# Performance work log

Measured on AMD Instinct MI355X. Metric: run time of the kernel, lower is better.

## Reference

```python
import jax, jax.numpy as jnp
import numpy as np

B, N_BUG, D_BUG, K, L, P = 2048, 2000, 30, 20, 40, 2
OMEGA_TEMP = 1.0


def setup_inputs() -> dict:
    key = jax.random.key(0)
    ks = jax.random.split(key, 14)
    f = lambda k, s, sc=1.0: sc * jax.random.normal(k, s, dtype=jnp.float32)
    return {
        "x": f(ks[0], (B, N_BUG)),
        "microbe_locs": f(ks[1], (N_BUG, D_BUG)),
        "mu_bug": f(ks[2], (L, D_BUG)),
        "r_bug": jax.random.uniform(ks[3], (L,), dtype=jnp.float32) * 20.0 + 10.0,
        "alpha": f(ks[4], (L, K)),
        "beta": f(ks[5], (K,)),
        "W1": f(ks[6], (K, L, P, 16), 0.5),
        "b1": f(ks[7], (K, L, P, 16), 0.1),
        "W2": f(ks[8], (K, L, P, 16, 16), 0.25),
        "b2": f(ks[9], (K, L, P, 16), 0.1),
        "W3": f(ks[10], (K, L, P, 16, 8), 0.25),
        "b3": f(ks[11], (K, L, P, 8), 0.1),
        "W4": f(ks[12], (K, L, P, 8), 0.35),
        "b4": f(ks[13], (K, L, P), 0.1),
    }


def reference(x, microbe_locs, mu_bug, r_bug, alpha, beta,
              W1, b1, W2, b2, W3, b3, W4, b4):
    # Distance-based soft microbe->cluster assignment (mu/r kernel):
    # kappa[m,l] = ||microbe_locs[m] - mu_bug[l]||^2
    kappa = jnp.sum((microbe_locs[:, None, :] - mu_bug[None, :, :]) ** 2, axis=-1)  # [N_bug, L]
    w_act = jax.nn.sigmoid((r_bug[None, :] - kappa) / OMEGA_TEMP)                  # [N_bug, L]
    g = x @ w_act                                                                   # [B, L] per-cluster microbe sums

    alpha_act = jax.nn.sigmoid(alpha)  # [L, K] soft edge selection

    # NAM: K*L*P independent tiny MLPs 1->16->16->8->1, batched over (k,l,p).
    h1 = jax.nn.elu(g[:, None, :, None, None] * W1[None] + b1[None])          # [B,K,L,P,16]
    h2 = jax.nn.elu(jnp.einsum('bklpi,klpij->bklpj', h1, W2) + b2[None])      # [B,K,L,P,16]
    h3 = jax.nn.elu(jnp.einsum('bklpi,klpij->bklpj', h2, W3) + b3[None])      # [B,K,L,P,8]
    f_out = jnp.einsum('bklpi,klpi->bklp', h3, W4) + b4[None]                 # [B,K,L,P]

    # out[b,k] = beta[k] + sum_l alpha_act[l,k] * sum_p f_out[b,k,l,p]
    out = beta[None, :] + jnp.einsum('bklp,lk->bk', f_out, alpha_act)         # [B,K]
    return out
```

## Files before the change

### kernel.cpp

```cpp
#include <hip/hip_runtime.h>
#include <hip/hip_bf16.h>

#define B_SZ 2048
#define NB   2000
#define DB   30
#define KK   20
#define LL   40
#define PP   2

#define BLOB_F 336

#define GRID_K1 880

typedef _Float16 f16x4 __attribute__((ext_vector_type(4)));
typedef float    f32x4 __attribute__((ext_vector_type(4)));

__device__ __forceinline__ float sigmoidf_fast(float z) {
    return 1.0f / (1.0f + __expf(-z));
}
__device__ __forceinline__ float eluf(float x) {
    return x > 0.0f ? x : (__expf(x) - 1.0f);
}

__global__ __launch_bounds__(256) void k1_prep(
    const float* __restrict__ locs, const float* __restrict__ mu,
    const float* __restrict__ r, const float* __restrict__ alpha,
    const float* __restrict__ beta,
    const float* __restrict__ W1, const float* __restrict__ b1,
    const float* __restrict__ W2, const float* __restrict__ b2,
    const float* __restrict__ W3, const float* __restrict__ b3,
    const float* __restrict__ W4, const float* __restrict__ b4,
    float* __restrict__ w_act, float* __restrict__ blob,
    float* __restrict__ g_T, float* __restrict__ out)
{
    __shared__ float smem[LL * DB + LL];
    const int tid  = threadIdx.x;
    const int bidx = blockIdx.x;
    const int vt   = bidx * 256 + tid;

    for (int j = vt; j < LL * B_SZ; j += GRID_K1 * 256) g_T[j] = 0.0f;

    if (bidx < 320) {
        for (int t = tid; t < LL * DB; t += 256) smem[t] = mu[t];
        if (tid < LL) smem[LL * DB + tid] = r[tid];
        __syncthreads();
        if (vt < NB * LL) {
            int m = vt / LL;
            int l = vt - m * LL;
            float kappa = 0.0f;
            #pragma unroll
            for (int d = 0; d < DB; ++d) {
                float diff = locs[m * DB + d] - smem[l * DB + d];
                kappa += diff * diff;
            }
            w_act[vt] = sigmoidf_fast(smem[LL * DB + l] - kappa);
        }
    } else if (bidx < 720) {
        int vt2 = vt - 320 * 256;
        int bidb = vt2 >> 6;
        int t = vt2 & 63;
        int k = bidb / (PP * LL);
        int rem = bidb - k * (PP * LL);
        int p = rem / LL;
        int l = rem - p * LL;
        int iw = (k * LL + l) * PP + p;
        int n = t & 15, q = t >> 4;
        float* o = blob + (size_t)bidb * BLOB_F;
        float aact = sigmoidf_fast(alpha[l * KK + k]);
        if (t < 16) {
            o[t]      = W1[iw * 16 + t];
            o[16 + t] = b1[iw * 16 + t];
            o[32 + t] = b2[iw * 16 + t];
            o[48 + t] = (t < 8) ? b3[iw * 8 + t] : 0.0f;
            o[64 + t] = (t < 8) ? W4[iw * 8 + t] * aact : 0.0f;
        }
        _Float16* w2a = (_Float16*)(o + 80);
        #pragma unroll
        for (int j = 0; j < 4; ++j)
            w2a[t * 4 + j] = (_Float16)W2[iw * 256 + (4 * q + j) * 16 + n];
        _Float16* w3a = (_Float16*)(o + 208);
        #pragma unroll
        for (int j = 0; j < 4; ++j)
            w3a[t * 4 + j] = (n < 8) ? (_Float16)W3[iw * 128 + (4 * q + j) * 8 + n]
                                     : (_Float16)0.0f;
    } else {
        if (tid < KK) {
            int k = tid;
            float s = beta[k];
            for (int l = 0; l < LL; ++l) {
                float a = sigmoidf_fast(alpha[l * KK + k]);
                s += a * (b4[(k * LL + l) * PP + 0] + b4[(k * LL + l) * PP + 1]);
            }
            smem[tid] = s;
        }
        __syncthreads();
        int gid = (bidx - 720) * 256 + tid;
        out[gid] = smem[gid % KK];
    }
}

__global__ __launch_bounds__(256) void k2_g(
    const float* __restrict__ x,
    const float* __restrict__ w_act,
    float* __restrict__ g_T)
{
    __shared__ float xs[64 * 125];

    int bb = blockIdx.x >> 4;
    int mq = blockIdx.x & 15;
    int tid = threadIdx.x;
    int i = tid & 63;
    int wu = __builtin_amdgcn_readfirstlane(tid >> 6);

    for (int t = tid; t < 64 * 125; t += 256) {
        int ii = t / 125;
        int jj = t - ii * 125;
        xs[t] = x[(bb * 64 + ii) * NB + mq * 125 + jj];
    }
    __syncthreads();

    const float* wrow = w_act + (mq * 125) * LL + wu * 10;
    const float* xrow = xs + i * 125;

    float acc[10];
    #pragma unroll
    for (int u = 0; u < 10; ++u) acc[u] = 0.0f;

    #pragma unroll 5
    for (int m = 0; m < 125; ++m) {
        float xv = xrow[m];
        #pragma unroll
        for (int u = 0; u < 10; ++u)
            acc[u] = fmaf(xv, wrow[m * LL + u], acc[u]);
    }

    #pragma unroll
    for (int u = 0; u < 10; ++u)
        atomicAdd(&g_T[(wu * 10 + u) * B_SZ + bb * 64 + i], acc[u]);
}

__global__ __launch_bounds__(256, 4) void k3_nam(
    const float* __restrict__ g_T,
    const float* __restrict__ blob,
    float* __restrict__ out)
{
    __shared__ __align__(16) float sw[10 * BLOB_F];

    int bid = blockIdx.x;
    int bb = bid & 7;
    int lc = (bid >> 3) & 3;
    int p  = (bid >> 5) & 1;
    int k  = bid >> 6;
    int tid = threadIdx.x;

    const int wv = tid >> 6, lane = tid & 63;
    const int n = lane & 15, q = lane >> 4;
    int b0 = bb * 256 + wv * 64 + n;

    float gc[4];
    #pragma unroll
    for (int g = 0; g < 4; ++g)
        gc[g] = g_T[(lc * 10) * B_SZ + b0 + 16 * g];

    {
        const float4* bl4 = (const float4*)blob;
        float4* sw4 = (float4*)sw;
        int base = ((k * PP + p) * LL + lc * 10) * (BLOB_F / 4);
        for (int t = tid; t < 10 * (BLOB_F / 4); t += 256)
            sw4[t] = bl4[base + t];
    }
    __syncthreads();

    float acc[4] = {0.0f, 0.0f, 0.0f, 0.0f};

    #pragma unroll 1
    for (int u = 0; u < 10; ++u) {
        float gn[4];
        if (u < 9) {
            #pragma unroll
            for (int g = 0; g < 4; ++g)
                gn[g] = g_T[(lc * 10 + u + 1) * B_SZ + b0 + 16 * g];
        }

        const float* W = sw + u * BLOB_F;
        f32x4 w1q = *(const f32x4*)(W + q * 4);
        f32x4 b1q = *(const f32x4*)(W + 16 + q * 4);
        f32x4 b2q = *(const f32x4*)(W + 32 + q * 4);
        f32x4 b3q = *(const f32x4*)(W + 48 + q * 4);
        f32x4 w4q = *(const f32x4*)(W + 64 + q * 4);
        f16x4 w2a = *(const f16x4*)((const _Float16*)(W + 80) + lane * 4);
        f16x4 w3a = *(const f16x4*)((const _Float16*)(W + 208) + lane * 4);

        f16x4 hb[4];
        #pragma unroll
        for (int g = 0; g < 4; ++g) {
            #pragma unroll
            for (int j = 0; j < 4; ++j)
                hb[g][j] = (_Float16)eluf(fmaf(gc[g], w1q[j], b1q[j]));
        }

        f32x4 d2[4];
        #pragma unroll
        for (int g = 0; g < 4; ++g)
            d2[g] = __builtin_amdgcn_mfma_f32_16x16x16f16(w2a, hb[g], b2q, 0, 0, 0);

        f16x4 hc[4];
        #pragma unroll
        for (int g = 0; g < 4; ++g) {
            #pragma unroll
            for (int j = 0; j < 4; ++j)
                hc[g][j] = (_Float16)eluf(d2[g][j]);
        }

        f32x4 d3[4];
        #pragma unroll
        for (int g = 0; g < 4; ++g)
            d3[g] = __builtin_amdgcn_mfma_f32_16x16x16f16(w3a, hc[g], b3q, 0, 0, 0);

        #pragma unroll
        for (int g = 0; g < 4; ++g) {
            #pragma unroll
            for (int rj = 0; rj < 4; ++rj)
                acc[g] = fmaf(eluf(d3[g][rj]), w4q[rj], acc[g]);
        }

        #pragma unroll
        for (int g = 0; g < 4; ++g) gc[g] = gn[g];
    }

    #pragma unroll
    for (int g = 0; g < 4; ++g) {
        acc[g] += __shfl_xor(acc[g], 16, 64);
        acc[g] += __shfl_xor(acc[g], 32, 64);
    }
    if (lane < 16) {
        #pragma unroll
        for (int g = 0; g < 4; ++g)
            atomicAdd(&out[(b0 + 16 * g) * KK + k], acc[g]);
    }
}

extern "C" void kernel_launch(void* const* d_in, const int* in_sizes, int n_in,
                              void* d_out, int out_size, void* d_ws, size_t ws_size,
                              hipStream_t stream) {
    const float* x     = (const float*)d_in[0];
    const float* locs  = (const float*)d_in[1];
    const float* mu    = (const float*)d_in[2];
    const float* r     = (const float*)d_in[3];
    const float* alpha = (const float*)d_in[4];
    const float* beta  = (const float*)d_in[5];
    const float* W1    = (const float*)d_in[6];
    const float* b1    = (const float*)d_in[7];
    const float* W2    = (const float*)d_in[8];
    const float* b2    = (const float*)d_in[9];
    const float* W3    = (const float*)d_in[10];
    const float* b3    = (const float*)d_in[11];
    const float* W4    = (const float*)d_in[12];
    const float* b4    = (const float*)d_in[13];
    float* out = (float*)d_out;

    float* ws0   = (float*)d_ws;
    float* w_act = ws0;
    float* g_T   = w_act + NB * LL;
    float* blob  = g_T + LL * B_SZ;

    k1_prep<<<GRID_K1, 256, 0, stream>>>(locs, mu, r, alpha, beta,
                                         W1, b1, W2, b2, W3, b3, W4, b4,
                                         w_act, blob, g_T, out);
    k2_g<<<512, 256, 0, stream>>>(x, w_act, g_T);
    k3_nam<<<1280, 256, 0, stream>>>(g_T, blob, out);
}
```

Measured before the change: 146.2 us.

## Fuse w_act computation into g GEMM and replace atomics with partial-sum reduction

Merges the separate prep and g-GEMM kernels into one launch. Each GEMM block now computes its own slice of the sigmoid distance weights into shared memory instead of reading a global w_act. Per-slice partial sums are written to a g_part buffer, which the NAM kernel reduces while staging them into shared memory, replacing the zero-init and atomicAdd accumulation. This removes one kernel launch and the atomics. In exchange, w_act is recomputed redundantly across the 32 batch tiles, fewer blocks do the GEMM, and every NAM block performs an 8-way reduction.

```diff
diff --git a/kernel.cpp b/kernel.cpp
--- a/kernel.cpp
+++ b/kernel.cpp
@@ -10,7 +10,7 @@
 
 #define BLOB_F 336
 
-#define GRID_K1 880
+#define NMQ 8
 
 typedef _Float16 f16x4 __attribute__((ext_vector_type(4)));
 typedef float    f32x4 __attribute__((ext_vector_type(4)));
@@ -22,41 +22,78 @@
     return x > 0.0f ? x : (__expf(x) - 1.0f);
 }
 
-__global__ __launch_bounds__(256) void k1_prep(
-    const float* __restrict__ locs, const float* __restrict__ mu,
-    const float* __restrict__ r, const float* __restrict__ alpha,
-    const float* __restrict__ beta,
+__global__ __launch_bounds__(256) void kA(
+    const float* __restrict__ x, const float* __restrict__ locs,
+    const float* __restrict__ mu, const float* __restrict__ r,
+    const float* __restrict__ alpha, const float* __restrict__ beta,
     const float* __restrict__ W1, const float* __restrict__ b1,
     const float* __restrict__ W2, const float* __restrict__ b2,
     const float* __restrict__ W3, const float* __restrict__ b3,
     const float* __restrict__ W4, const float* __restrict__ b4,
-    float* __restrict__ w_act, float* __restrict__ blob,
-    float* __restrict__ g_T, float* __restrict__ out)
+    float* __restrict__ g_part, float* __restrict__ blob,
+    float* __restrict__ out)
 {
-    __shared__ float smem[LL * DB + LL];
     const int tid  = threadIdx.x;
     const int bidx = blockIdx.x;
-    const int vt   = bidx * 256 + tid;
-
-    for (int j = vt; j < LL * B_SZ; j += GRID_K1 * 256) g_T[j] = 0.0f;
-
-    if (bidx < 320) {
-        for (int t = tid; t < LL * DB; t += 256) smem[t] = mu[t];
-        if (tid < LL) smem[LL * DB + tid] = r[tid];
-        __syncthreads();
-        if (vt < NB * LL) {
-            int m = vt / LL;
-            int l = vt - m * LL;
-            float kappa = 0.0f;
-            #pragma unroll
-            for (int d = 0; d < DB; ++d) {
-                float diff = locs[m * DB + d] - smem[l * DB + d];
-                kappa += diff * diff;
-            }
-            w_act[vt] = sigmoidf_fast(smem[LL * DB + l] - kappa);
-        }
-    } else if (bidx < 720) {
-        int vt2 = vt - 320 * 256;
+
+    if (bidx < 256) {
+        __shared__ float xs[64 * 125];
+        __shared__ float ws[4 * 125 * 10];
+
+        int bb = bidx >> 3;
+        int mq = bidx & 7;
+        int i  = tid & 63;
+        int wu = __builtin_amdgcn_readfirstlane(tid >> 6);
+        float* wsw = ws + wu * 1250;
+
+        float acc[10];
+        #pragma unroll
+        for (int u = 0; u < 10; ++u) acc[u] = 0.0f;
+
+        for (int c = 0; c < 2; ++c) {
+            int m0 = mq * 250 + c * 125;
+            __syncthreads();
+            for (int t = tid; t < 64 * 125; t += 256) {
+                int ii = t / 125;
+                int jj = t - ii * 125;
+                xs[t] = x[(bb * 64 + ii) * NB + m0 + jj];
+            }
+            #pragma unroll
+            for (int rr = 0; rr < 2; ++rr) {
+                int m = rr * 64 + i;
+                if (m < 125) {
+                    float lv[DB];
+                    #pragma unroll
+                    for (int d = 0; d < DB; ++d)
+                        lv[d] = locs[(m0 + m) * DB + d];
+                    #pragma unroll 1
+                    for (int u = 0; u < 10; ++u) {
+                        int l = wu * 10 + u;
+                        float kap = 0.0f;
+                        #pragma unroll
+                        for (int d = 0; d < DB; ++d) {
+                            float df = lv[d] - mu[l * DB + d];
+                            kap = fmaf(df, df, kap);
+                        }
+                        wsw[m * 10 + u] = sigmoidf_fast(r[l] - kap);
+                    }
+                }
+            }
+            __syncthreads();
+            #pragma unroll 5
+            for (int m = 0; m < 125; ++m) {
+                float xv = xs[i * 125 + m];
+                #pragma unroll
+                for (int u = 0; u < 10; ++u)
+                    acc[u] = fmaf(xv, wsw[m * 10 + u], acc[u]);
+            }
+        }
+        #pragma unroll
+        for (int u = 0; u < 10; ++u)
+            g_part[(mq * LL + wu * 10 + u) * B_SZ + bb * 64 + i] = acc[u];
+
+    } else if (bidx < 656) {
+        int vt2 = (bidx - 256) * 256 + tid;
         int bidb = vt2 >> 6;
         int t = vt2 & 63;
         int k = bidb / (PP * LL);
@@ -84,6 +121,7 @@
             w3a[t * 4 + j] = (n < 8) ? (_Float16)W3[iw * 128 + (4 * q + j) * 8 + n]
                                      : (_Float16)0.0f;
     } else {
+        __shared__ float sbeta[KK];
         if (tid < KK) {
             int k = tid;
             float s = beta[k];
@@ -91,60 +129,21 @@
                 float a = sigmoidf_fast(alpha[l * KK + k]);
                 s += a * (b4[(k * LL + l) * PP + 0] + b4[(k * LL + l) * PP + 1]);
             }
-            smem[tid] = s;
+            sbeta[k] = s;
         }
         __syncthreads();
-        int gid = (bidx - 720) * 256 + tid;
-        out[gid] = smem[gid % KK];
-    }
-}
-
-__global__ __launch_bounds__(256) void k2_g(
-    const float* __restrict__ x,
-    const float* __restrict__ w_act,
-    float* __restrict__ g_T)
-{
-    __shared__ float xs[64 * 125];
-
-    int bb = blockIdx.x >> 4;
-    int mq = blockIdx.x & 15;
-    int tid = threadIdx.x;
-    int i = tid & 63;
-    int wu = __builtin_amdgcn_readfirstlane(tid >> 6);
-
-    for (int t = tid; t < 64 * 125; t += 256) {
-        int ii = t / 125;
-        int jj = t - ii * 125;
-        xs[t] = x[(bb * 64 + ii) * NB + mq * 125 + jj];
-    }
-    __syncthreads();
-
-    const float* wrow = w_act + (mq * 125) * LL + wu * 10;
-    const float* xrow = xs + i * 125;
-
-    float acc[10];
-    #pragma unroll
-    for (int u = 0; u < 10; ++u) acc[u] = 0.0f;
-
-    #pragma unroll 5
-    for (int m = 0; m < 125; ++m) {
-        float xv = xrow[m];
-        #pragma unroll
-        for (int u = 0; u < 10; ++u)
-            acc[u] = fmaf(xv, wrow[m * LL + u], acc[u]);
-    }
-
-    #pragma unroll
-    for (int u = 0; u < 10; ++u)
-        atomicAdd(&g_T[(wu * 10 + u) * B_SZ + bb * 64 + i], acc[u]);
-}
-
-__global__ __launch_bounds__(256, 4) void k3_nam(
-    const float* __restrict__ g_T,
+        int gid = (bidx - 656) * 256 + tid;
+        out[gid] = sbeta[gid % KK];
+    }
+}
+
+__global__ __launch_bounds__(256, 4) void kB(
+    const float* __restrict__ g_part,
     const float* __restrict__ blob,
     float* __restrict__ out)
 {
     __shared__ __align__(16) float sw[10 * BLOB_F];
+    __shared__ __align__(16) float gbuf[10 * 256];
 
     int bid = blockIdx.x;
     int bb = bid & 7;
@@ -153,15 +152,6 @@
     int k  = bid >> 6;
     int tid = threadIdx.x;
 
-    const int wv = tid >> 6, lane = tid & 63;
-    const int n = lane & 15, q = lane >> 4;
-    int b0 = bb * 256 + wv * 64 + n;
-
-    float gc[4];
-    #pragma unroll
-    for (int g = 0; g < 4; ++g)
-        gc[g] = g_T[(lc * 10) * B_SZ + b0 + 16 * g];
-
     {
         const float4* bl4 = (const float4*)blob;
         float4* sw4 = (float4*)sw;
@@ -169,19 +159,31 @@
         for (int t = tid; t < 10 * (BLOB_F / 4); t += 256)
             sw4[t] = bl4[base + t];
     }
+    {
+        const float4* gp4 = (const float4*)g_part;
+        float4* gb4 = (float4*)gbuf;
+        for (int e = tid; e < 640; e += 256) {
+            int u  = e >> 6;
+            int jj = e & 63;
+            float4 s = {0.0f, 0.0f, 0.0f, 0.0f};
+            #pragma unroll
+            for (int mq = 0; mq < NMQ; ++mq) {
+                float4 v = gp4[(mq * LL + lc * 10 + u) * (B_SZ / 4) + bb * 64 + jj];
+                s.x += v.x; s.y += v.y; s.z += v.z; s.w += v.w;
+            }
+            gb4[e] = s;
+        }
+    }
     __syncthreads();
+
+    const int wv = tid >> 6, lane = tid & 63;
+    const int n = lane & 15, q = lane >> 4;
+    int b0 = bb * 256 + wv * 64 + n;
 
     float acc[4] = {0.0f, 0.0f, 0.0f, 0.0f};
 
     #pragma unroll 1
     for (int u = 0; u < 10; ++u) {
-        float gn[4];
-        if (u < 9) {
-            #pragma unroll
-            for (int g = 0; g < 4; ++g)
-                gn[g] = g_T[(lc * 10 + u + 1) * B_SZ + b0 + 16 * g];
-        }
-
         const float* W = sw + u * BLOB_F;
         f32x4 w1q = *(const f32x4*)(W + q * 4);
         f32x4 b1q = *(const f32x4*)(W + 16 + q * 4);
@@ -191,6 +193,11 @@
         f16x4 w2a = *(const f16x4*)((const _Float16*)(W + 80) + lane * 4);
         f16x4 w3a = *(const f16x4*)((const _Float16*)(W + 208) + lane * 4);
 
+        float gc[4];
+        #pragma unroll
+        for (int g = 0; g < 4; ++g)
+            gc[g] = gbuf[u * 256 + wv * 64 + 16 * g + n];
+
         f16x4 hb[4];
         #pragma unroll
         for (int g = 0; g < 4; ++g) {
@@ -223,9 +230,6 @@
             for (int rj = 0; rj < 4; ++rj)
                 acc[g] = fmaf(eluf(d3[g][rj]), w4q[rj], acc[g]);
         }
-
-        #pragma unroll
-        for (int g = 0; g < 4; ++g) gc[g] = gn[g];
     }
 
     #pragma unroll
@@ -259,14 +263,12 @@
     const float* b4    = (const float*)d_in[13];
     float* out = (float*)d_out;
 
-    float* ws0   = (float*)d_ws;
-    float* w_act = ws0;
-    float* g_T   = w_act + NB * LL;
-    float* blob  = g_T + LL * B_SZ;
-
-    k1_prep<<<GRID_K1, 256, 0, stream>>>(locs, mu, r, alpha, beta,
-                                         W1, b1, W2, b2, W3, b3, W4, b4,
-                                         w_act, blob, g_T, out);
-    k2_g<<<512, 256, 0, stream>>>(x, w_act, g_T);
-    k3_nam<<<1280, 256, 0, stream>>>(g_T, blob, out);
-}
+    float* ws0    = (float*)d_ws;
+    float* g_part = ws0;
+    float* blob   = g_part + (size_t)NMQ * LL * B_SZ;
+
+    kA<<<816, 256, 0, stream>>>(x, locs, mu, r, alpha, beta,
+                                W1, b1, W2, b2, W3, b3, W4, b4,
+                                g_part, blob, out);
+    kB<<<1280, 256, 0, stream>>>(g_part, blob, out);
+}
```

Result: slower. 151.0 us (+3.3%).
